# Performance work log

Hardware: AMD Instinct MI355X
Metric: run time of the kernel (lower is better)

Reference implementation:

```python
import jax, jax.numpy as jnp
import numpy as np

N = 50000        # nodes
E = 800000       # edges (before self-loops)
NFEAT = 256
NHID = 32
HEADS = 8
NOUT = 128
NEG_SLOPE = 0.2
EPS = 1e-5


def _gat_layer(x, src, dst, W, att_src, att_dst, bias, heads, ch, concat):
    """PyG-style GATConv (shared weights for src/dst, self-loops already appended)."""
    n = x.shape[0]
    h = (x @ W).reshape(n, heads, ch)                      # [N,H,C]
    a_src = (h * att_src).sum(-1)                          # [N,H]
    a_dst = (h * att_dst).sum(-1)                          # [N,H]
    e = jax.nn.leaky_relu(a_src[src] + a_dst[dst], NEG_SLOPE)  # [E',H]
    # segment softmax over incoming edges of each dst node
    m = jax.ops.segment_max(e, dst, num_segments=n)        # [N,H]
    m = jnp.where(jnp.isfinite(m), m, 0.0)
    ex = jnp.exp(e - m[dst])                               # [E',H]
    denom = jax.ops.segment_sum(ex, dst, num_segments=n)   # [N,H]
    alpha = ex / (denom[dst] + 1e-16)                      # [E',H]
    msg = h[src] * alpha[:, :, None]                       # [E',H,C]
    out = jax.ops.segment_sum(msg, dst, num_segments=n)    # [N,H,C]
    out = out.reshape(n, heads * ch) if concat else out.mean(axis=1)
    return out + bias


def setup_inputs() -> dict:
    key = jax.random.key(0)
    ks = jax.random.split(key, 14)
    s = 0.05
    return {
        "x": jax.random.normal(ks[0], (N, NFEAT), jnp.float32),
        "edge_index": jax.random.randint(ks[1], (2, E), 0, N, dtype=jnp.int64),
        "W1": jax.random.normal(ks[2], (NFEAT, HEADS * NHID), jnp.float32) * s,
        "att_src1": jax.random.normal(ks[3], (HEADS, NHID), jnp.float32) * s,
        "att_dst1": jax.random.normal(ks[4], (HEADS, NHID), jnp.float32) * s,
        "b1": jnp.zeros((HEADS * NHID,), jnp.float32),
        "W2": jax.random.normal(ks[5], (HEADS * NHID, NOUT), jnp.float32) * s,
        "att_src2": jax.random.normal(ks[6], (1, NOUT), jnp.float32) * s,
        "att_dst2": jax.random.normal(ks[7], (1, NOUT), jnp.float32) * s,
        "b2": jnp.zeros((NOUT,), jnp.float32),
        "bn_gamma": jnp.ones((NOUT,), jnp.float32),
        "bn_beta": jnp.zeros((NOUT,), jnp.float32),
        "ln_gamma": jnp.ones((NOUT,), jnp.float32),
        "ln_beta": jnp.zeros((NOUT,), jnp.float32),
    }


def reference(x, edge_index, W1, att_src1, att_dst1, b1, W2, att_src2, att_dst2, b2,
              bn_gamma, bn_beta, ln_gamma, ln_beta):
    loops = jnp.arange(N, dtype=edge_index.dtype)
    src = jnp.concatenate([edge_index[0], loops])
    dst = jnp.concatenate([edge_index[1], loops])
    # layer 1: concat heads, then relu (dropout is identity at inference)
    h = jax.nn.relu(_gat_layer(x, src, dst, W1, att_src1, att_dst1, b1, HEADS, NHID, True))
    # layer 2: single head, mean (no concat), relu
    h = jax.nn.relu(_gat_layer(h, src, dst, W2, att_src2, att_dst2, b2, 1, NOUT, False))
    # BatchNorm1d with batch statistics (biased var, eps=1e-5)
    mu = h.mean(axis=0)
    var = h.var(axis=0)
    h = (h - mu) / jnp.sqrt(var + EPS) * bn_gamma + bn_beta
    # LayerNorm over last dim
    mu2 = h.mean(axis=-1, keepdims=True)
    var2 = h.var(axis=-1, keepdims=True)
    return (h - mu2) / jnp.sqrt(var2 + EPS) * ln_gamma + ln_beta
```

## Files before the change

kernel.cpp:

```cpp
#include <hip/hip_runtime.h>
#include <cstdint>
#include <cstddef>

#define HEADS   8
#define NFEAT   256
#define NOUT    128
#define NEG     0.2f
#define EPSV    1e-5f

typedef unsigned short ushort_t;
typedef __attribute__((ext_vector_type(8))) short s8v;
typedef __attribute__((ext_vector_type(4))) float f4v;

static __device__ __forceinline__ float lrelu(float x) { return x > 0.f ? x : NEG * x; }

static __device__ __forceinline__ float bf2f(ushort_t u) {
    union { unsigned int i; float f; } v; v.i = ((unsigned int)u) << 16; return v.f;
}
static __device__ __forceinline__ ushort_t f2bf(float f) {
    union { float f; unsigned int i; } v; v.f = f;
    unsigned int x = v.i;
    return (ushort_t)((x + 0x7fff + ((x >> 16) & 1)) >> 16);
}
static __device__ __forceinline__ float bits2f(unsigned int u) {
    union { unsigned int i; float f; } v; v.i = u; return v.f;
}
static __device__ __forceinline__ unsigned int f2bits(float f) {
    union { float f; unsigned int i; } v; v.f = f; return v.i;
}

static __device__ __forceinline__ int detect64(const int* __restrict__ ei, int E) {
    int lane = threadIdx.x & 63;
    long idx = 2L * ((long)lane * (E / 64)) + 1;
    int v = ei[idx];
    unsigned long long ball = __ballot(v == 0);
    return (ball == ~0ull) ? 1 : 0;
}

__global__ void k_prep(const int* __restrict__ ei, int* __restrict__ counts,
                       int E, int n, int cblocks,
                       const float* __restrict__ W1, const float* __restrict__ W2,
                       ushort_t* __restrict__ Wh1, ushort_t* __restrict__ Wl1,
                       ushort_t* __restrict__ Wh2, ushort_t* __restrict__ Wl2) {
    if (blockIdx.x < (unsigned)cblocks) {
        int is64 = detect64(ei, E);
        int i = blockIdx.x * 256 + threadIdx.x;
        if (i < E) {
            int d = ei[(size_t)(E + i) << is64];
            atomicAdd(&counts[d], 1);
        } else if (i < E + n) {
            atomicAdd(&counts[i - E], 1);
        }
    } else {
        int gid = (blockIdx.x - cblocks) * 256 + threadIdx.x;
        const float* W; ushort_t* Wh; ushort_t* Wl; int M;
        if (gid < 256 * 256) { W = W1; Wh = Wh1; Wl = Wl1; M = 256; }
        else { gid -= 256 * 256; if (gid >= 256 * 128) return; W = W2; Wh = Wh2; Wl = Wl2; M = 128; }
        int k = gid / M, nn = gid - k * M;
        int ntile = nn >> 4, j = nn & 15, kc = k >> 3, e = k & 7;
        int p = ((ntile * 32 + kc) * 16 + j) * 8 + e;
        float v = W[(size_t)k * M + nn];
        ushort_t hi = f2bf(v);
        float r = v - bf2f(hi);
        Wh[p] = hi;
        Wl[p] = f2bf(r);
    }
}

__global__ __launch_bounds__(1024) void k_scan1(const int* __restrict__ counts,
                                                int* __restrict__ incl,
                                                int* __restrict__ bsum, int n) {
    int t = threadIdx.x, i = blockIdx.x * 1024 + t;
    int lane = t & 63, w = t >> 6;
    int v = (i < n) ? counts[i] : 0;
    int sv = v;
#pragma unroll
    for (int o = 1; o < 64; o <<= 1) { int u = __shfl_up(sv, o, 64); if (lane >= o) sv += u; }
    __shared__ int wsum[16];
    if (lane == 63) wsum[w] = sv;
    __syncthreads();
    if (w == 0) {
        int bs = (lane < 16) ? wsum[lane] : 0;
#pragma unroll
        for (int o = 1; o < 16; o <<= 1) { int u = __shfl_up(bs, o, 64); if (lane >= o) bs += u; }
        if (lane < 16) wsum[lane] = bs;
    }
    __syncthreads();
    int pre = (w > 0) ? wsum[w - 1] : 0;
    sv += pre;
    if (i < n) incl[i] = sv;
    if (t == 1023) bsum[blockIdx.x] = sv;
}

__global__ void k_scan3(const int* __restrict__ incl, const int* __restrict__ bsum,
                        const int* __restrict__ counts,
                        int* __restrict__ offs, int* __restrict__ cursor, int n) {
    __shared__ int pre_s;
    int chunk = blockIdx.x >> 2;
    if (threadIdx.x == 0) {
        int s = 0;
        for (int j = 0; j < chunk; ++j) s += bsum[j];
        pre_s = s;
    }
    __syncthreads();
    int i = blockIdx.x * 256 + threadIdx.x;
    if (i < n) {
        int v = incl[i] + pre_s;
        offs[i + 1] = v;
        cursor[i] = v - counts[i];
    }
    if (i == 0) offs[0] = 0;
}

__global__ void k_fill(const int* __restrict__ ei, int* __restrict__ cursor,
                       int* __restrict__ esrc, int E, int n) {
    int is64 = detect64(ei, E);
    int i = blockIdx.x * blockDim.x + threadIdx.x;
    if (i >= E + n) return;
    int s, d;
    if (i < E) { s = ei[(size_t)i << is64]; d = ei[(size_t)(E + i) << is64]; }
    else       { s = i - E; d = s; }
    int p = atomicAdd(&cursor[d], 1);
    esrc[p] = s;
}

template <int MOUT>
__global__ __launch_bounds__(256) void k_mm(const float* __restrict__ A,
                                            const ushort_t* __restrict__ Wh,
                                            const ushort_t* __restrict__ Wl,
                                            ushort_t* __restrict__ C,
                                            const float* __restrict__ att_s,
                                            const float* __restrict__ att_d,
                                            float* __restrict__ as_o,
                                            float* __restrict__ ad_o, int n) {
    __shared__ ushort_t Ah[64][40];
    __shared__ ushort_t Al[64][40];
    const int t = threadIdx.x;
    const int lane = t & 63, w = t >> 6;
    const int r0 = blockIdx.x * 64;
    const int srow = t >> 2;
    const int kh = (t & 3) * 8;
    const int arow = r0 + srow;
    const bool rowok = arow < n;

    f4v acc[4][2];
#pragma unroll
    for (int a = 0; a < 4; ++a)
#pragma unroll
        for (int b = 0; b < 2; ++b) { f4v z = {0.f, 0.f, 0.f, 0.f}; acc[a][b] = z; }

    float pre[8];
    const float* abase = &A[(size_t)arow * 256 + kh];
#pragma unroll
    for (int q = 0; q < 2; ++q) {
        float4 v = rowok ? *reinterpret_cast<const float4*>(abase + q * 4)
                         : float4{0.f, 0.f, 0.f, 0.f};
        pre[q * 4 + 0] = v.x; pre[q * 4 + 1] = v.y;
        pre[q * 4 + 2] = v.z; pre[q * 4 + 3] = v.w;
    }

    const int lj = lane & 15, lk = lane >> 4;

    for (int kb = 0; kb < 256; kb += 32) {
        __syncthreads();
        {
            unsigned int hw[4], lw[4];
#pragma unroll
            for (int p = 0; p < 4; ++p) {
                unsigned int x0 = f2bits(pre[p * 2]);
                unsigned int x1 = f2bits(pre[p * 2 + 1]);
                unsigned int h1b = x1 & 0xffff0000u;
                float lo0 = pre[p * 2] - bits2f(x0 & 0xffff0000u);
                float lo1 = pre[p * 2 + 1] - bits2f(h1b);
                hw[p] = (x0 >> 16) | h1b;
                lw[p] = (f2bits(lo0) >> 16) | (f2bits(lo1) & 0xffff0000u);
            }
            uint4 hv = {hw[0], hw[1], hw[2], hw[3]};
            uint4 lv = {lw[0], lw[1], lw[2], lw[3]};
            *reinterpret_cast<uint4*>(&Ah[srow][kh]) = hv;
            *reinterpret_cast<uint4*>(&Al[srow][kh]) = lv;
        }
        __syncthreads();
        if (kb < 224) {
            const float* ap = abase + kb + 32;
#pragma unroll
            for (int q = 0; q < 2; ++q) {
                float4 v = rowok ? *reinterpret_cast<const float4*>(ap + q * 4)
                                 : float4{0.f, 0.f, 0.f, 0.f};
                pre[q * 4 + 0] = v.x; pre[q * 4 + 1] = v.y;
                pre[q * 4 + 2] = v.z; pre[q * 4 + 3] = v.w;
            }
        }
        const int kc0 = kb >> 3;
        s8v ah[4], al[4];
#pragma unroll
        for (int mf = 0; mf < 4; ++mf) {
            ah[mf] = *reinterpret_cast<const s8v*>(&Ah[mf * 16 + lj][lk * 8]);
            al[mf] = *reinterpret_cast<const s8v*>(&Al[mf * 16 + lj][lk * 8]);
        }
#pragma unroll
        for (int nf = 0; nf < 2; ++nf) {
            int ntile = (MOUT == 256 ? blockIdx.y * 8 : 0) + w * 2 + nf;
            size_t boff = ((size_t)(ntile * 32 + kc0 + lk) * 16 + lj) * 8;
            s8v bh = *reinterpret_cast<const s8v*>(&Wh[boff]);
            s8v bl = *reinterpret_cast<const s8v*>(&Wl[boff]);
#pragma unroll
            for (int mf = 0; mf < 4; ++mf) {
                acc[mf][nf] = __builtin_amdgcn_mfma_f32_16x16x32_bf16(ah[mf], bh, acc[mf][nf], 0, 0, 0);
                acc[mf][nf] = __builtin_amdgcn_mfma_f32_16x16x32_bf16(ah[mf], bl, acc[mf][nf], 0, 0, 0);
                acc[mf][nf] = __builtin_amdgcn_mfma_f32_16x16x32_bf16(al[mf], bh, acc[mf][nf], 0, 0, 0);
            }
        }
    }

    const int colw = (MOUT == 256 ? blockIdx.y * 128 : 0) + w * 32;

#pragma unroll
    for (int mf = 0; mf < 4; ++mf) {
        int rr = r0 + mf * 16 + lk * 4;
#pragma unroll
        for (int nf = 0; nf < 2; ++nf) {
            int cc = colw + nf * 16 + lj;
#pragma unroll
            for (int r = 0; r < 4; ++r) {
                if (rr + r < n) C[(size_t)(rr + r) * MOUT + cc] = f2bf(acc[mf][nf][r]);
            }
        }
    }

    float asv[2], adv[2];
#pragma unroll
    for (int nf = 0; nf < 2; ++nf) {
        asv[nf] = att_s[colw + nf * 16 + lj];
        adv[nf] = att_d[colw + nf * 16 + lj];
    }
#pragma unroll
    for (int mf = 0; mf < 4; ++mf) {
        int rr = r0 + mf * 16 + lk * 4;
#pragma unroll
        for (int r = 0; r < 4; ++r) {
            float ss = acc[mf][0][r] * asv[0] + acc[mf][1][r] * asv[1];
            float sd = acc[mf][0][r] * adv[0] + acc[mf][1][r] * adv[1];
#pragma unroll
            for (int o = 1; o < 16; o <<= 1) {
                ss += __shfl_xor(ss, o, 64); sd += __shfl_xor(sd, o, 64);
            }
            if (lj == 0 && rr + r < n) {
                if (MOUT == 256) {
                    int head = (colw >> 5);
                    as_o[(size_t)(rr + r) * 8 + head] = ss;
                    ad_o[(size_t)(rr + r) * 8 + head] = sd;
                } else {
                    atomicAdd(&as_o[rr + r], ss);
                    atomicAdd(&ad_o[rr + r], sd);
                }
            }
        }
    }
}

__global__ __launch_bounds__(128) void k_agg1(const ushort_t* __restrict__ h1,
                                              const float* __restrict__ as1,
                                              const float* __restrict__ ad1,
                                              const int* __restrict__ offs,
                                              const int* __restrict__ esrc,
                                              const float* __restrict__ b1,
                                              float* __restrict__ out1, int n, int tot) {
    int wid = (blockIdx.x * 128 + threadIdx.x) >> 6;
    int lane = threadIdx.x & 63;
    if (wid >= n) return;
    int e0 = offs[wid], e1 = offs[wid + 1];
    int deg = e1 - e0;

    if (deg <= 64) {
        const int l = lane & 31;
        const int h = lane >> 5;
        const int hd = l >> 2;
        const int cb = l * 8;

        int ei_idx = e0 + lane;
        int es = esrc[ei_idx < tot ? ei_idx : (tot - 1)];

        const int headA = lane >> 3, g = lane & 7;
        float adnA = ad1[(size_t)wid * 8 + headA];
        float a[8];
#pragma unroll
        for (int k = 0; k < 8; ++k) {
            int i = g + 8 * k;
            int s = __shfl(es, i, 64);
            a[k] = (i < deg) ? as1[(size_t)s * 8 + headA] : -1e30f;
        }
        float mx = a[0];
#pragma unroll
        for (int k = 1; k < 8; ++k) mx = fmaxf(mx, a[k]);
#pragma unroll
        for (int o = 1; o < 8; o <<= 1) mx = fmaxf(mx, __shfl_xor(mx, o, 64));
        float mA = lrelu(mx + adnA);
#pragma unroll
        for (int k = 0; k < 8; ++k)
            a[k] = __expf(lrelu(a[k] + adnA) - mA);

        float d = 0.f;
        float ac0 = 0.f, ac1 = 0.f, ac2 = 0.f, ac3 = 0.f;
        float ac4 = 0.f, ac5 = 0.f, ac6 = 0.f, ac7 = 0.f;
#pragma unroll
        for (int u = 0; u < 8; ++u) {
            if (8 * u < deg) {
#pragma unroll
                for (int v = 0; v < 4; ++v) {
                    int i = 8 * u + 2 * v + h;
                    int s = __shfl(es, i, 64);
                    float p = __shfl(a[u], hd * 8 + 2 * v + h, 64);
                    if (i < deg) {
                        uint4 hv = *reinterpret_cast<const uint4*>(&h1[(size_t)s * 256 + cb]);
                        d += p;
                        ac0 += p * bits2f(hv.x << 16);
                        ac1 += p * bits2f(hv.x & 0xffff0000u);
                        ac2 += p * bits2f(hv.y << 16);
                        ac3 += p * bits2f(hv.y & 0xffff0000u);
                        ac4 += p * bits2f(hv.z << 16);
                        ac5 += p * bits2f(hv.z & 0xffff0000u);
                        ac6 += p * bits2f(hv.w << 16);
                        ac7 += p * bits2f(hv.w & 0xffff0000u);
                    }
                }
            }
        }
        d   += __shfl_xor(d, 32, 64);
        ac0 += __shfl_xor(ac0, 32, 64); ac1 += __shfl_xor(ac1, 32, 64);
        ac2 += __shfl_xor(ac2, 32, 64); ac3 += __shfl_xor(ac3, 32, 64);
        ac4 += __shfl_xor(ac4, 32, 64); ac5 += __shfl_xor(ac5, 32, 64);
        ac6 += __shfl_xor(ac6, 32, 64); ac7 += __shfl_xor(ac7, 32, 64);
        if (lane < 32) {
            float inv = 1.f / (d + 1e-16f);
            float4 b0 = *reinterpret_cast<const float4*>(&b1[cb]);
            float4 b4 = *reinterpret_cast<const float4*>(&b1[cb + 4]);
            float4 o0, o1;
            o0.x = fmaxf(ac0 * inv + b0.x, 0.f);
            o0.y = fmaxf(ac1 * inv + b0.y, 0.f);
            o0.z = fmaxf(ac2 * inv + b0.z, 0.f);
            o0.w = fmaxf(ac3 * inv + b0.w, 0.f);
            o1.x = fmaxf(ac4 * inv + b4.x, 0.f);
            o1.y = fmaxf(ac5 * inv + b4.y, 0.f);
            o1.z = fmaxf(ac6 * inv + b4.z, 0.f);
            o1.w = fmaxf(ac7 * inv + b4.w, 0.f);
            *reinterpret_cast<float4*>(&out1[(size_t)wid * 256 + cb]) = o0;
            *reinterpret_cast<float4*>(&out1[(size_t)wid * 256 + cb + 4]) = o1;
        }
    } else {
        int head = lane >> 3;
        int g = lane & 7;
        int cb = lane * 4;
        float adn = ad1[(size_t)wid * 8 + head];
        float mx = -1e30f;
        for (int e = e0 + g; e < e1; e += 8)
            mx = fmaxf(mx, as1[(size_t)esrc[e] * 8 + head]);
#pragma unroll
        for (int o = 1; o < 8; o <<= 1) mx = fmaxf(mx, __shfl_xor(mx, o, 64));
        float m = lrelu(mx + adn);
        float d = 0.f, ax = 0.f, ay = 0.f, az = 0.f, aw = 0.f;
        for (int e = e0; e < e1; ++e) {
            int s = esrc[e];
            float p = __expf(lrelu(as1[(size_t)s * 8 + head] + adn) - m);
            ushort4 hv = *reinterpret_cast<const ushort4*>(&h1[(size_t)s * 256 + cb]);
            d += p;
            ax += p * bf2f(hv.x);
            ay += p * bf2f(hv.y);
            az += p * bf2f(hv.z);
            aw += p * bf2f(hv.w);
        }
        float inv = 1.f / (d + 1e-16f);
        float4 bb = *reinterpret_cast<const float4*>(&b1[cb]);
        float4 o;
        o.x = fmaxf(ax * inv + bb.x, 0.f);
        o.y = fmaxf(ay * inv + bb.y, 0.f);
        o.z = fmaxf(az * inv + bb.z, 0.f);
        o.w = fmaxf(aw * inv + bb.w, 0.f);
        *reinterpret_cast<float4*>(&out1[(size_t)wid * 256 + cb]) = o;
    }
}

__global__ __launch_bounds__(128) void k_agg2(const ushort_t* __restrict__ h2,
                                              const float* __restrict__ as2,
                                              const float* __restrict__ ad2,
                                              const int* __restrict__ offs,
                                              const int* __restrict__ esrc,
                                              const float* __restrict__ b2,
                                              float* __restrict__ out2, int n, int tot) {
    int wid = (blockIdx.x * 128 + threadIdx.x) >> 6;
    int lane = threadIdx.x & 63;
    if (wid >= n) return;
    float adn = ad2[wid];
    int e0 = offs[wid], e1 = offs[wid + 1];
    int deg = e1 - e0;

    if (deg <= 64) {
        const int l = lane & 15;
        const int q = lane >> 4;
        const int cb = l * 8;

        int ei_idx = e0 + lane;
        int es = esrc[ei_idx < tot ? ei_idx : (tot - 1)];
        float av0 = (lane < deg) ? as2[es] : -1e30f;
        float mx = av0;
#pragma unroll
        for (int o = 1; o < 64; o <<= 1) mx = fmaxf(mx, __shfl_xor(mx, o, 64));
        float m = lrelu(mx + adn);
        float p0 = __expf(lrelu(av0 + adn) - m);

        float d = 0.f;
        float ac0 = 0.f, ac1 = 0.f, ac2 = 0.f, ac3 = 0.f;
        float ac4 = 0.f, ac5 = 0.f, ac6 = 0.f, ac7 = 0.f;
#pragma unroll
        for (int u = 0; u < 4; ++u) {
            if (16 * u < deg) {
#pragma unroll
                for (int v = 0; v < 4; ++v) {
                    int i = 16 * u + 4 * v + q;
                    int s = __shfl(es, i, 64);
                    float p = __shfl(p0, i, 64);
                    if (i < deg) {
                        uint4 hv = *reinterpret_cast<const uint4*>(&h2[(size_t)s * 128 + cb]);
                        d += p;
                        ac0 += p * bits2f(hv.x << 16);
                        ac1 += p * bits2f(hv.x & 0xffff0000u);
                        ac2 += p * bits2f(hv.y << 16);
                        ac3 += p * bits2f(hv.y & 0xffff0000u);
                        ac4 += p * bits2f(hv.z << 16);
                        ac5 += p * bits2f(hv.z & 0xffff0000u);
                        ac6 += p * bits2f(hv.w << 16);
                        ac7 += p * bits2f(hv.w & 0xffff0000u);
                    }
                }
            }
        }
#pragma unroll
        for (int o = 16; o <= 32; o <<= 1) {
            d   += __shfl_xor(d, o, 64);
            ac0 += __shfl_xor(ac0, o, 64); ac1 += __shfl_xor(ac1, o, 64);
            ac2 += __shfl_xor(ac2, o, 64); ac3 += __shfl_xor(ac3, o, 64);
            ac4 += __shfl_xor(ac4, o, 64); ac5 += __shfl_xor(ac5, o, 64);
            ac6 += __shfl_xor(ac6, o, 64); ac7 += __shfl_xor(ac7, o, 64);
        }
        if (lane < 16) {
            float inv = 1.f / (d + 1e-16f);
            float4 b0 = *reinterpret_cast<const float4*>(&b2[cb]);
            float4 b4 = *reinterpret_cast<const float4*>(&b2[cb + 4]);
            float4 o0, o1;
            o0.x = fmaxf(ac0 * inv + b0.x, 0.f);
            o0.y = fmaxf(ac1 * inv + b0.y, 0.f);
            o0.z = fmaxf(ac2 * inv + b0.z, 0.f);
            o0.w = fmaxf(ac3 * inv + b0.w, 0.f);
            o1.x = fmaxf(ac4 * inv + b4.x, 0.f);
            o1.y = fmaxf(ac5 * inv + b4.y, 0.f);
            o1.z = fmaxf(ac6 * inv + b4.z, 0.f);
            o1.w = fmaxf(ac7 * inv + b4.w, 0.f);
            *reinterpret_cast<float4*>(&out2[(size_t)wid * 128 + cb]) = o0;
            *reinterpret_cast<float4*>(&out2[(size_t)wid * 128 + cb + 4]) = o1;
        }
    } else {
        int cb = lane * 2;
        float mx = -1e30f;
        for (int e = e0 + lane; e < e1; e += 64)
            mx = fmaxf(mx, as2[esrc[e]]);
#pragma unroll
        for (int o = 1; o < 64; o <<= 1) mx = fmaxf(mx, __shfl_xor(mx, o, 64));
        float m = lrelu(mx + adn);
        float d = 0.f, ax = 0.f, ay = 0.f;
        for (int e = e0; e < e1; ++e) {
            int s = esrc[e];
            float p = __expf(lrelu(as2[s] + adn) - m);
            ushort2 hv = *reinterpret_cast<const ushort2*>(&h2[(size_t)s * 128 + cb]);
            d += p;
            ax += p * bf2f(hv.x);
            ay += p * bf2f(hv.y);
        }
        float inv = 1.f / (d + 1e-16f);
        float o0 = fmaxf(ax * inv + b2[cb], 0.f);
        float o1 = fmaxf(ay * inv + b2[cb + 1], 0.f);
        float2 o = {o0, o1};
        *reinterpret_cast<float2*>(&out2[(size_t)wid * 128 + cb]) = o;
    }
}

__global__ __launch_bounds__(128) void k_bnstat(const float* __restrict__ out2,
                                                float* __restrict__ bnsum,
                                                float* __restrict__ bnsq, int n) {
    int c = threadIdx.x;
    float s = 0.f, q = 0.f;
    for (int r = blockIdx.x; r < n; r += gridDim.x) {
        float v = out2[(size_t)r * 128 + c];
        s += v;
        q += v * v;
    }
    atomicAdd(&bnsum[c], s);
    atomicAdd(&bnsq[c], q);
}

__global__ __launch_bounds__(256) void k_final(const float* __restrict__ out2,
                                               const float* __restrict__ bnsum,
                                               const float* __restrict__ bnsq,
                                               const float* __restrict__ bng,
                                               const float* __restrict__ bnb,
                                               const float* __restrict__ lng,
                                               const float* __restrict__ lnb,
                                               float* __restrict__ out, int n) {
    int wid = (blockIdx.x * blockDim.x + threadIdx.x) >> 6;
    int lane = threadIdx.x & 63;
    if (wid >= n) return;
    int c0 = lane, c1 = lane + 64;
    float invn = 1.f / (float)n;
    float mu0 = bnsum[c0] * invn, mu1 = bnsum[c1] * invn;
    float v0 = bnsq[c0] * invn - mu0 * mu0;
    float v1 = bnsq[c1] * invn - mu1 * mu1;
    float r0 = rsqrtf(v0 + EPSV), r1 = rsqrtf(v1 + EPSV);
    float x0 = out2[(size_t)wid * 128 + c0];
    float x1 = out2[(size_t)wid * 128 + c1];
    float y0 = (x0 - mu0) * r0 * bng[c0] + bnb[c0];
    float y1 = (x1 - mu1) * r1 * bng[c1] + bnb[c1];
    float s = y0 + y1, q = y0 * y0 + y1 * y1;
#pragma unroll
    for (int o = 1; o < 64; o <<= 1) { s += __shfl_xor(s, o, 64); q += __shfl_xor(q, o, 64); }
    float mu = s * (1.f / 128.f);
    float var = q * (1.f / 128.f) - mu * mu;
    float rr = rsqrtf(var + EPSV);
    out[(size_t)wid * 128 + c0] = (y0 - mu) * rr * lng[c0] + lnb[c0];
    out[(size_t)wid * 128 + c1] = (y1 - mu) * rr * lng[c1] + lnb[c1];
}

extern "C" void kernel_launch(void* const* d_in, const int* in_sizes, int n_in,
                              void* d_out, int out_size, void* d_ws, size_t ws_size,
                              hipStream_t stream) {
    const float* x    = (const float*)d_in[0];
    const int*   ei   = (const int*)d_in[1];
    const float* W1   = (const float*)d_in[2];
    const float* ats1 = (const float*)d_in[3];
    const float* atd1 = (const float*)d_in[4];
    const float* b1   = (const float*)d_in[5];
    const float* W2   = (const float*)d_in[6];
    const float* ats2 = (const float*)d_in[7];
    const float* atd2 = (const float*)d_in[8];
    const float* b2   = (const float*)d_in[9];
    const float* bng  = (const float*)d_in[10];
    const float* bnb  = (const float*)d_in[11];
    const float* lng  = (const float*)d_in[12];
    const float* lnb  = (const float*)d_in[13];

    const int n = in_sizes[0] / NFEAT;
    const int E = in_sizes[1] / 2;
    const int tot = E + n;

    auto align = [](size_t v) { return (v + 255) & ~(size_t)255; };
    char* ws = (char*)d_ws;
    size_t off = 0;
    ushort_t* h1 = (ushort_t*)(ws + off); off += align((size_t)n * 256 * 2);
    float* out1 = (float*)(ws + off); off += align((size_t)n * 256 * 4);
    ushort_t* h2 = h1;
    float* out2 = out1;
    float* as1 = (float*)(ws + off); off += align((size_t)n * 8 * 4);
    float* ad1 = (float*)(ws + off); off += align((size_t)n * 8 * 4);
    int* counts = (int*)(ws + off); off += align((size_t)n * 12 + 1024);
    float* bnsum = (float*)(counts + n);
    float* bnsq  = bnsum + 128;
    float* as2   = bnsq + 128;
    float* ad2   = as2 + n;
    int* offs   = (int*)(ws + off); off += align((size_t)(n + 1) * 4);
    int* cursor = (int*)(ws + off); off += align((size_t)n * 4);
    int* esrc   = (int*)(ws + off); off += align((size_t)tot * 4);
    int* incl   = (int*)(ws + off); off += align((size_t)n * 4);
    int* bsum   = (int*)(ws + off); off += align(64 * 4);
    ushort_t* Wh1 = (ushort_t*)(ws + off); off += align((size_t)256 * 256 * 2);
    ushort_t* Wl1 = (ushort_t*)(ws + off); off += align((size_t)256 * 256 * 2);
    ushort_t* Wh2 = (ushort_t*)(ws + off); off += align((size_t)256 * 128 * 2);
    ushort_t* Wl2 = (ushort_t*)(ws + off); off += align((size_t)256 * 128 * 2);

    hipMemsetAsync(counts, 0, (size_t)n * 12 + 1024, stream);

    const int cblocks = (tot + 255) / 256;
    const int pblocks = (256 * 256 + 256 * 128 + 255) / 256;
    k_prep<<<cblocks + pblocks, 256, 0, stream>>>(ei, counts, E, n, cblocks,
                                                  W1, W2, Wh1, Wl1, Wh2, Wl2);
    int nsb = (n + 1023) / 1024;
    k_scan1<<<nsb, 1024, 0, stream>>>(counts, incl, bsum, n);
    k_scan3<<<(n + 255) / 256, 256, 0, stream>>>(incl, bsum, counts, offs, cursor, n);
    k_fill<<<(tot + 255) / 256, 256, 0, stream>>>(ei, cursor, esrc, E, n);

    const int gx = (n + 63) / 64;
    k_mm<256><<<dim3(gx, 2), 256, 0, stream>>>(x, Wh1, Wl1, h1, ats1, atd1, as1, ad1, n);
    k_agg1<<<(n + 1) / 2, 128, 0, stream>>>(h1, as1, ad1, offs, esrc, b1, out1, n, tot);

    k_mm<128><<<dim3(gx, 1), 256, 0, stream>>>(out1, Wh2, Wl2, h2, ats2, atd2, as2, ad2, n);
    k_agg2<<<(n + 1) / 2, 128, 0, stream>>>(h2, as2, ad2, offs, esrc, b2, out2, n, tot);

    k_bnstat<<<512, 128, 0, stream>>>(out2, bnsum, bnsq, n);
    k_final<<<(n + 3) / 4, 256, 0, stream>>>(out2, bnsum, bnsq, bng, bnb, lng, lnb,
                                             (float*)d_out, n);
}
```

Baseline: 339.9 us.

## Double-buffer LDS tiles and prefetch weight fragments in MFMA GEMM

The GEMM kernel moves from a single LDS buffer to two, so it needs one barrier per k-step instead of two. The next A tile is converted to split-bf16 and staged into the alternate buffer while the current buffer feeds the MFMAs. Weight fragments for the next step are also prefetched into registers. This costs more LDS and registers, which could lower occupancy. The GEMM is only part of the total GNN pipeline time.

```diff
diff --git a/kernel.cpp b/kernel.cpp
--- a/kernel.cpp
+++ b/kernel.cpp
@@ -133,8 +133,8 @@
                                             const float* __restrict__ att_d,
                                             float* __restrict__ as_o,
                                             float* __restrict__ ad_o, int n) {
-    __shared__ ushort_t Ah[64][40];
-    __shared__ ushort_t Al[64][40];
+    __shared__ ushort_t Ah[2][64][40];
+    __shared__ ushort_t Al[2][64][40];
     const int t = threadIdx.x;
     const int lane = t & 63, w = t >> 6;
     const int r0 = blockIdx.x * 64;
@@ -142,6 +142,7 @@
     const int kh = (t & 3) * 8;
     const int arow = r0 + srow;
     const bool rowok = arow < n;
+    const int lj = lane & 15, lk = lane >> 4;
 
     f4v acc[4][2];
 #pragma unroll
@@ -149,8 +150,70 @@
 #pragma unroll
         for (int b = 0; b < 2; ++b) { f4v z = {0.f, 0.f, 0.f, 0.f}; acc[a][b] = z; }
 
+    const float* abase = &A[(size_t)arow * 256 + kh];
     float pre[8];
-    const float* abase = &A[(size_t)arow * 256 + kh];
+
+#define MM_STAGE(BUF)                                                         \
+    {                                                                         \
+        unsigned int hw[4], lw[4];                                            \
+        _Pragma("unroll")                                                     \
+        for (int p = 0; p < 4; ++p) {                                         \
+            unsigned int x0 = f2bits(pre[p * 2]);                             \
+            unsigned int x1 = f2bits(pre[p * 2 + 1]);                         \
+            unsigned int h1b = x1 & 0xffff0000u;                              \
+            float lo0 = pre[p * 2] - bits2f(x0 & 0xffff0000u);                \
+            float lo1 = pre[p * 2 + 1] - bits2f(h1b);                         \
+            hw[p] = (x0 >> 16) | h1b;                                         \
+            lw[p] = (f2bits(lo0) >> 16) | (f2bits(lo1) & 0xffff0000u);        \
+        }                                                                     \
+        uint4 hv = {hw[0], hw[1], hw[2], hw[3]};                              \
+        uint4 lv = {lw[0], lw[1], lw[2], lw[3]};                              \
+        *reinterpret_cast<uint4*>(&Ah[BUF][srow][kh]) = hv;                   \
+        *reinterpret_cast<uint4*>(&Al[BUF][srow][kh]) = lv;                   \
+    }
+
+#define MM_LOADB(KB, BH, BL)                                                  \
+    {                                                                         \
+        const int kc0_ = (KB) >> 3;                                           \
+        _Pragma("unroll")                                                     \
+        for (int nf = 0; nf < 2; ++nf) {                                      \
+            int ntile = (MOUT == 256 ? blockIdx.y * 8 : 0) + w * 2 + nf;      \
+            size_t boff = ((size_t)(ntile * 32 + kc0_ + lk) * 16 + lj) * 8;   \
+            BH[nf] = *reinterpret_cast<const s8v*>(&Wh[boff]);                \
+            BL[nf] = *reinterpret_cast<const s8v*>(&Wl[boff]);                \
+        }                                                                     \
+    }
+
+#define MM_STEP(KB, CUR, BH, BL, BHN, BLN)                                    \
+    {                                                                         \
+        if ((KB) < 224) {                                                     \
+            const float* ap = abase + (KB) + 32;                              \
+            _Pragma("unroll")                                                 \
+            for (int q = 0; q < 2; ++q) {                                     \
+                float4 v = rowok ? *reinterpret_cast<const float4*>(ap + q*4) \
+                                 : float4{0.f, 0.f, 0.f, 0.f};                \
+                pre[q*4+0]=v.x; pre[q*4+1]=v.y; pre[q*4+2]=v.z; pre[q*4+3]=v.w; \
+            }                                                                 \
+            MM_LOADB((KB) + 32, BHN, BLN);                                    \
+        }                                                                     \
+        s8v ah[4], al[4];                                                     \
+        _Pragma("unroll")                                                     \
+        for (int mf = 0; mf < 4; ++mf) {                                      \
+            ah[mf] = *reinterpret_cast<const s8v*>(&Ah[CUR][mf*16+lj][lk*8]); \
+            al[mf] = *reinterpret_cast<const s8v*>(&Al[CUR][mf*16+lj][lk*8]); \
+        }                                                                     \
+        _Pragma("unroll")                                                     \
+        for (int nf = 0; nf < 2; ++nf)                                        \
+            _Pragma("unroll")                                                 \
+            for (int mf = 0; mf < 4; ++mf) {                                  \
+                acc[mf][nf] = __builtin_amdgcn_mfma_f32_16x16x32_bf16(ah[mf], BH[nf], acc[mf][nf], 0, 0, 0); \
+                acc[mf][nf] = __builtin_amdgcn_mfma_f32_16x16x32_bf16(ah[mf], BL[nf], acc[mf][nf], 0, 0, 0); \
+                acc[mf][nf] = __builtin_amdgcn_mfma_f32_16x16x32_bf16(al[mf], BH[nf], acc[mf][nf], 0, 0, 0); \
+            }                                                                 \
+        if ((KB) < 224) MM_STAGE((CUR) ^ 1);                                  \
+        __syncthreads();                                                      \
+    }
+
 #pragma unroll
     for (int q = 0; q < 2; ++q) {
         float4 v = rowok ? *reinterpret_cast<const float4*>(abase + q * 4)
@@ -158,59 +221,14 @@
         pre[q * 4 + 0] = v.x; pre[q * 4 + 1] = v.y;
         pre[q * 4 + 2] = v.z; pre[q * 4 + 3] = v.w;
     }
-
-    const int lj = lane & 15, lk = lane >> 4;
-
-    for (int kb = 0; kb < 256; kb += 32) {
-        __syncthreads();
-        {
-            unsigned int hw[4], lw[4];
-#pragma unroll
-            for (int p = 0; p < 4; ++p) {
-                unsigned int x0 = f2bits(pre[p * 2]);
-                unsigned int x1 = f2bits(pre[p * 2 + 1]);
-                unsigned int h1b = x1 & 0xffff0000u;
-                float lo0 = pre[p * 2] - bits2f(x0 & 0xffff0000u);
-                float lo1 = pre[p * 2 + 1] - bits2f(h1b);
-                hw[p] = (x0 >> 16) | h1b;
-                lw[p] = (f2bits(lo0) >> 16) | (f2bits(lo1) & 0xffff0000u);
-            }
-            uint4 hv = {hw[0], hw[1], hw[2], hw[3]};
-            uint4 lv = {lw[0], lw[1], lw[2], lw[3]};
-            *reinterpret_cast<uint4*>(&Ah[srow][kh]) = hv;
-            *reinterpret_cast<uint4*>(&Al[srow][kh]) = lv;
-        }
-        __syncthreads();
-        if (kb < 224) {
-            const float* ap = abase + kb + 32;
-#pragma unroll
-            for (int q = 0; q < 2; ++q) {
-                float4 v = rowok ? *reinterpret_cast<const float4*>(ap + q * 4)
-                                 : float4{0.f, 0.f, 0.f, 0.f};
-                pre[q * 4 + 0] = v.x; pre[q * 4 + 1] = v.y;
-                pre[q * 4 + 2] = v.z; pre[q * 4 + 3] = v.w;
-            }
-        }
-        const int kc0 = kb >> 3;
-        s8v ah[4], al[4];
-#pragma unroll
-        for (int mf = 0; mf < 4; ++mf) {
-            ah[mf] = *reinterpret_cast<const s8v*>(&Ah[mf * 16 + lj][lk * 8]);
-            al[mf] = *reinterpret_cast<const s8v*>(&Al[mf * 16 + lj][lk * 8]);
-        }
-#pragma unroll
-        for (int nf = 0; nf < 2; ++nf) {
-            int ntile = (MOUT == 256 ? blockIdx.y * 8 : 0) + w * 2 + nf;
-            size_t boff = ((size_t)(ntile * 32 + kc0 + lk) * 16 + lj) * 8;
-            s8v bh = *reinterpret_cast<const s8v*>(&Wh[boff]);
-            s8v bl = *reinterpret_cast<const s8v*>(&Wl[boff]);
-#pragma unroll
-            for (int mf = 0; mf < 4; ++mf) {
-                acc[mf][nf] = __builtin_amdgcn_mfma_f32_16x16x32_bf16(ah[mf], bh, acc[mf][nf], 0, 0, 0);
-                acc[mf][nf] = __builtin_amdgcn_mfma_f32_16x16x32_bf16(ah[mf], bl, acc[mf][nf], 0, 0, 0);
-                acc[mf][nf] = __builtin_amdgcn_mfma_f32_16x16x32_bf16(al[mf], bh, acc[mf][nf], 0, 0, 0);
-            }
-        }
+    s8v bhA[2], blA[2], bhB[2], blB[2];
+    MM_LOADB(0, bhA, blA);
+    MM_STAGE(0);
+    __syncthreads();
+
+    for (int kb = 0; kb < 256; kb += 64) {
+        MM_STEP(kb,      0, bhA, blA, bhB, blB);
+        MM_STEP(kb + 32, 1, bhB, blB, bhA, blA);
     }
 
     const int colw = (MOUT == 256 ? blockIdx.y * 128 : 0) + w * 32;
@@ -257,6 +275,9 @@
             }
         }
     }
+#undef MM_STEP
+#undef MM_LOADB
+#undef MM_STAGE
 }
 
 __global__ __launch_bounds__(128) void k_agg1(const ushort_t* __restrict__ h1,
```

Measured after the change: 333.2 us. 1.02x faster.
